# Performance work log

Hardware: AMD Instinct MI355X
Metric: run time of the kernel (lower is better)

Reference implementation:

```python
import jax, jax.numpy as jnp
import numpy as np

N_USERS = 100000
N_ITEMS = 50000
N_NODES = N_USERS + N_ITEMS
NNZ = 4800000
DIM = 64
N_HOPS = 3
EPS = 0.1
PERTURBED = True


def setup_inputs() -> dict:
    key = jax.random.key(0)
    k1, k2, k3, k4, k5 = jax.random.split(key, 5)
    user_embed = jax.random.normal(k1, (N_USERS, DIM), dtype=jnp.float32) * 0.1
    item_embed = jax.random.normal(k2, (N_ITEMS, DIM), dtype=jnp.float32) * 0.1
    adj_rows = jax.random.randint(k3, (NNZ,), 0, N_NODES, dtype=jnp.int32)
    adj_cols = jax.random.randint(k4, (NNZ,), 0, N_NODES, dtype=jnp.int32)
    # scale values ~ 1/avg_degree so repeated propagation stays well-conditioned
    adj_vals = jax.random.uniform(k5, (NNZ,), dtype=jnp.float32) * (1.0 / 32.0)
    return {"user_embed": user_embed, "item_embed": item_embed,
            "adj_rows": adj_rows, "adj_cols": adj_cols, "adj_vals": adj_vals}


def _spmm(rows, cols, vals, x):
    # sparse [N,N] @ dense [N,D] via gather + segment-sum
    msgs = vals[:, None] * x[cols]  # [nnz, D]
    return jax.ops.segment_sum(msgs, rows, num_segments=N_NODES)


def _forward(user_embed, item_embed, adj_rows, adj_cols, adj_vals):
    ego = jnp.concatenate([user_embed, item_embed], axis=0)  # [N, D]
    noise_key = jax.random.key(42)
    all_embeddings = []
    layer_embeddings = ego
    for k in range(N_HOPS):
        ego = _spmm(adj_rows, adj_cols, adj_vals, ego)
        if PERTURBED:
            noise = jax.random.uniform(jax.random.fold_in(noise_key, k), ego.shape, dtype=ego.dtype)
            noise = noise / jnp.linalg.norm(noise, axis=-1, keepdims=True)  # F.normalize dim=-1
            ego = ego + jnp.sign(ego) * noise * EPS
        all_embeddings.append(ego)
        if k == 0:
            layer_embeddings = ego
    all_mean = jnp.mean(jnp.stack(all_embeddings, axis=1), axis=1)  # [N, D]
    user_all, item_all = all_mean[:N_USERS], all_mean[N_USERS:]
    user_layer, item_layer = layer_embeddings[:N_USERS], layer_embeddings[N_USERS:]
    return (user_all, item_all, user_layer, item_layer)


def reference(user_embed, item_embed, adj_rows, adj_cols, adj_vals):
    return _forward(user_embed, item_embed, adj_rows, adj_cols, adj_vals)
```

## Files before the change

### kernel.cpp

```cpp
#include <hip/hip_runtime.h>
#include <stdint.h>

#define N_USERS 100000
#define N_ITEMS 50000
#define N_NODES 150000
#define NNZ     4800000
#define DIM     64
#define NELEM   (N_NODES * DIM)
#define EPS_F   0.1f


#define NBUCK  3072
#define RPB    49
#define BCAP   1856
#define CHUNK  8192
#define NCHUNK 586

#define E_MASK   0x7FFFFFu
#define COL_MASK 0x3FFFFu

typedef unsigned long long ull;

__host__ __device__ inline void threefry2x32_fn(unsigned k0, unsigned k1,
                                                unsigned x0, unsigned x1,
                                                unsigned* o0, unsigned* o1) {
  unsigned ks0 = k0, ks1 = k1, ks2 = k0 ^ k1 ^ 0x1BD11BDAu;
  x0 += ks0; x1 += ks1;
#define TF_ROUND(r) { x0 += x1; x1 = (x1 << (r)) | (x1 >> (32 - (r))); x1 ^= x0; }
  TF_ROUND(13) TF_ROUND(15) TF_ROUND(26) TF_ROUND(6)
  x0 += ks1; x1 += ks2 + 1u;
  TF_ROUND(17) TF_ROUND(29) TF_ROUND(16) TF_ROUND(24)
  x0 += ks2; x1 += ks0 + 2u;
  TF_ROUND(13) TF_ROUND(15) TF_ROUND(26) TF_ROUND(6)
  x0 += ks0; x1 += ks1 + 3u;
  TF_ROUND(17) TF_ROUND(29) TF_ROUND(16) TF_ROUND(24)
  x0 += ks1; x1 += ks2 + 4u;
  TF_ROUND(13) TF_ROUND(15) TF_ROUND(26) TF_ROUND(6)
  x0 += ks2; x1 += ks0 + 5u;
#undef TF_ROUND
  *o0 = x0; *o1 = x1;
}

__global__ void hist_kernel(const int* __restrict__ rows,
                            int* __restrict__ counts) {
  __shared__ int h[NBUCK];
  int c = blockIdx.x, tid = threadIdx.x;
  for (int t = tid; t < NBUCK; t += 256) h[t] = 0;
  __syncthreads();
  int cb = c * CHUNK;
  #pragma unroll 4
  for (int k = 0; k < CHUNK / 256; ++k) {
    int i = cb + k * 256 + tid;
    if (i < NNZ) {
      int r = rows[i];
      atomicAdd(&h[r / RPB], 1);
    }
  }
  __syncthreads();
  for (int t = tid; t < NBUCK; t += 256)
    counts[c * NBUCK + t] = h[t];
}

__global__ void scan_kernel(const int* __restrict__ counts,
                            int* __restrict__ base,
                            int* __restrict__ btot) {
  int b = blockIdx.x * 256 + threadIdx.x;
  int run = 0;
  #pragma unroll 8
  for (int c = 0; c < NCHUNK; ++c) {
    int v = counts[c * NBUCK + b];
    base[c * NBUCK + b] = run;
    run += v;
  }
  btot[b] = run;
}

__global__ void scatter_kernel(const int* __restrict__ rows,
                               const int* __restrict__ cols,
                               const int* __restrict__ base,
                               ull* __restrict__ staging) {
  __shared__ int cur[NBUCK];
  int c = blockIdx.x, tid = threadIdx.x;
  for (int t = tid; t < NBUCK; t += 256) cur[t] = base[c * NBUCK + t];
  __syncthreads();
  int cb = c * CHUNK;
  #pragma unroll 4
  for (int k = 0; k < CHUNK / 256; ++k) {
    int i = cb + k * 256 + tid;
    if (i < NNZ) {
      int r  = rows[i];
      int cc = cols[i];
      int b  = r / RPB;
      int lr = r - b * RPB;
      int p  = atomicAdd(&cur[b], 1);
      if (p < BCAP)
        staging[(long long)b * BCAP + p] =
            ((ull)(unsigned)lr << 41) | ((ull)(unsigned)cc << 23) | (unsigned)i;
    }
  }
}

__global__ void group_sort_kernel(const float* __restrict__ vals,
                                  const int* __restrict__ btot,
                                  ull* __restrict__ staging,
                                  int* __restrict__ cnt,
                                  int* __restrict__ off) {
  __shared__ ull B[BCAP];
  __shared__ int rowcnt[RPB];
  __shared__ int rowoff[RPB + 1];
  __shared__ int rowcur[RPB];
  int b = blockIdx.x, tid = threadIdx.x;
  int tot = btot[b]; if (tot > BCAP) tot = BCAP;
  ull* sg = staging + (long long)b * BCAP;

  for (int t = tid; t < RPB; t += 256) { rowcnt[t] = 0; rowcur[t] = 0; }
  __syncthreads();

  for (int s = tid; s < tot; s += 256) {
    ull v = sg[s];
    atomicAdd(&rowcnt[(int)(v >> 41)], 1);
  }
  __syncthreads();

  if (tid == 0) {
    int run = 0;
    for (int t = 0; t < RPB; ++t) { rowoff[t] = run; run += rowcnt[t]; }
    rowoff[RPB] = run;
  }
  __syncthreads();

  int row0 = b * RPB;
  for (int t = tid; t < RPB; t += 256) {
    int r = row0 + t;
    if (r < N_NODES) { cnt[r] = rowcnt[t]; off[r] = b * BCAP + rowoff[t]; }
  }

  for (int s = tid; s < tot; s += 256) {
    ull v = sg[s];
    int lr = (int)(v >> 41);
    int p = atomicAdd(&rowcur[lr], 1);
    B[rowoff[lr] + p] = v;
  }
  __syncthreads();

  for (int s = tid; s < tot; s += 256) {
    ull v = B[s];
    int lr = (int)(v >> 41);
    unsigned e = (unsigned)(v & E_MASK);
    int lo = rowoff[lr], hi = rowoff[lr + 1];
    int rk = 0;
    for (int j = lo; j < hi; ++j)
      rk += ((unsigned)(B[j] & E_MASK) < e) ? 1 : 0;
    float val = vals[e];
    unsigned col = (unsigned)((v >> 23) & COL_MASK);
    sg[lo + rk] = ((ull)col << 32) | __float_as_uint(val);
  }
}

template <int K>
__global__ void spmm_noise_kernel(const ull* __restrict__ pairs,
                                  const int* __restrict__ cnt,
                                  const int* __restrict__ off,
                                  const float* __restrict__ user_e,
                                  const float* __restrict__ item_e,
                                  const float* __restrict__ src,
                                  float* __restrict__ dst,
                                  float* __restrict__ out_mean,
                                  unsigned key0, unsigned key1) {
  int wid  = threadIdx.x >> 6;
  int lane = threadIdx.x & 63;
  int row  = blockIdx.x * 4 + wid;
  int row_u = __builtin_amdgcn_readfirstlane(row);
  int d = cnt[row_u];
  if (d > 128) d = 128;
  const ull* prow = pairs + off[row_u];

  #define GATHER(c, xout_) do {                                            \
    if (K == 0) {                                                          \
      const float* bp_ = ((c) < N_USERS)                                   \
          ? user_e + (long long)(c) * DIM                                  \
          : item_e + (long long)((c) - N_USERS) * DIM;                     \
      xout_ = bp_[lane];                                                   \
    } else {                                                               \
      xout_ = src[(long long)(c) * DIM + lane];                            \
    }                                                                      \
  } while (0)

  float acc = 0.0f;
  for (int t = 0; t < d; t += 8) {
    int i0 = t,     i1 = t + 1, i2 = t + 2, i3 = t + 3;
    int i4 = t + 4, i5 = t + 5, i6 = t + 6, i7 = t + 7;
    int dm1 = d - 1;
    if (i1 > dm1) i1 = dm1;  if (i2 > dm1) i2 = dm1;  if (i3 > dm1) i3 = dm1;
    if (i4 > dm1) i4 = dm1;  if (i5 > dm1) i5 = dm1;  if (i6 > dm1) i6 = dm1;
    if (i7 > dm1) i7 = dm1;
    ull p0 = prow[i0], p1 = prow[i1], p2 = prow[i2], p3 = prow[i3];
    ull p4 = prow[i4], p5 = prow[i5], p6 = prow[i6], p7 = prow[i7];
    int c0 = (int)(unsigned)(p0 >> 32), c1 = (int)(unsigned)(p1 >> 32);
    int c2 = (int)(unsigned)(p2 >> 32), c3 = (int)(unsigned)(p3 >> 32);
    int c4 = (int)(unsigned)(p4 >> 32), c5 = (int)(unsigned)(p5 >> 32);
    int c6 = (int)(unsigned)(p6 >> 32), c7 = (int)(unsigned)(p7 >> 32);
    float x0, x1, x2, x3, x4, x5, x6, x7;
    GATHER(c0, x0); GATHER(c1, x1); GATHER(c2, x2); GATHER(c3, x3);
    GATHER(c4, x4); GATHER(c5, x5); GATHER(c6, x6); GATHER(c7, x7);
    float v0 = __uint_as_float((unsigned)(p0 & 0xffffffffu));
    float v1 = (t + 1 < d) ? __uint_as_float((unsigned)(p1 & 0xffffffffu)) : 0.0f;
    float v2 = (t + 2 < d) ? __uint_as_float((unsigned)(p2 & 0xffffffffu)) : 0.0f;
    float v3 = (t + 3 < d) ? __uint_as_float((unsigned)(p3 & 0xffffffffu)) : 0.0f;
    float v4 = (t + 4 < d) ? __uint_as_float((unsigned)(p4 & 0xffffffffu)) : 0.0f;
    float v5 = (t + 5 < d) ? __uint_as_float((unsigned)(p5 & 0xffffffffu)) : 0.0f;
    float v6 = (t + 6 < d) ? __uint_as_float((unsigned)(p6 & 0xffffffffu)) : 0.0f;
    float v7 = (t + 7 < d) ? __uint_as_float((unsigned)(p7 & 0xffffffffu)) : 0.0f;
    acc = __fadd_rn(acc, __fmul_rn(v0, x0));
    acc = __fadd_rn(acc, __fmul_rn(v1, x1));
    acc = __fadd_rn(acc, __fmul_rn(v2, x2));
    acc = __fadd_rn(acc, __fmul_rn(v3, x3));
    acc = __fadd_rn(acc, __fmul_rn(v4, x4));
    acc = __fadd_rn(acc, __fmul_rn(v5, x5));
    acc = __fadd_rn(acc, __fmul_rn(v6, x6));
    acc = __fadd_rn(acc, __fmul_rn(v7, x7));
  }
  #undef GATHER

  int i = row * DIM + lane;
  unsigned o0, o1;
  threefry2x32_fn(key0, key1, 0u, (unsigned)i, &o0, &o1);
  unsigned bits = o0 ^ o1;
  float u = __uint_as_float((bits >> 9) | 0x3f800000u) - 1.0f;
  float ss = __fmul_rn(u, u);
  #pragma unroll
  for (int offs = 32; offs >= 1; offs >>= 1)
    ss += __shfl_xor(ss, offs, 64);
  float noise = u / sqrtf(ss);
  float s = (acc > 0.0f) ? 1.0f : ((acc < 0.0f) ? -1.0f : 0.0f);
  float val = __fadd_rn(acc, __fmul_rn(s, __fmul_rn(noise, EPS_F)));

  if (K == 0) {
    dst[i] = val;
    out_mean[i] = val;
  } else if (K == 1) {
    dst[i] = val;
    out_mean[i] = __fadd_rn(out_mean[i], val);
  } else {
    out_mean[i] = __fadd_rn(out_mean[i], val) / 3.0f;
  }
}

extern "C" void kernel_launch(void* const* d_in, const int* in_sizes, int n_in,
                              void* d_out, int out_size, void* d_ws, size_t ws_size,
                              hipStream_t stream) {
  const float* user_e = (const float*)d_in[0];
  const float* item_e = (const float*)d_in[1];
  const int*   rows   = (const int*)d_in[2];
  const int*   cols   = (const int*)d_in[3];
  const float* vals   = (const float*)d_in[4];

  float* out_mean  = (float*)d_out;
  float* out_layer = (float*)d_out + NELEM;

  char* w = (char*)d_ws;
  ull*   staging = (ull*)w;
  int*   counts  = (int*)(w + 45613056);
  int*   basep   = (int*)(w + 52813824);
  int*   btot    = (int*)(w + 60014592);
  int*   cnt     = (int*)(w + 60026880);
  int*   off     = (int*)(w + 60626880);
  float* ego     = (float*)(w + 61226880);

  unsigned hk0[3], hk1[3];
  for (int k = 0; k < 3; ++k)
    threefry2x32_fn(0u, 42u, 0u, (unsigned)k, &hk0[k], &hk1[k]);

  const int BT = 256;
  const unsigned row_blocks = N_NODES / 4;

  hist_kernel<<<NCHUNK, BT, 0, stream>>>(rows, counts);
  scan_kernel<<<NBUCK / BT, BT, 0, stream>>>(counts, basep, btot);
  scatter_kernel<<<NCHUNK, BT, 0, stream>>>(rows, cols, basep, staging);
  group_sort_kernel<<<NBUCK, BT, 0, stream>>>(vals, btot, staging, cnt, off);

  spmm_noise_kernel<0><<<row_blocks, BT, 0, stream>>>(
      staging, cnt, off, user_e, item_e, nullptr, out_layer, out_mean, hk0[0], hk1[0]);
  spmm_noise_kernel<1><<<row_blocks, BT, 0, stream>>>(
      staging, cnt, off, nullptr, nullptr, out_layer, ego, out_mean, hk0[1], hk1[1]);
  spmm_noise_kernel<2><<<row_blocks, BT, 0, stream>>>(
      staging, cnt, off, nullptr, nullptr, ego, nullptr, out_mean, hk0[2], hk1[2]);
}
```

Measured before the change: 910.0 us.

## Fuse histogram, scan and scatter into one kernel using global atomic bucket offsets

The separate histogram, per-bucket scan and scatter kernels become a single kernel. Each chunk block builds its local bucket histogram in shared memory, reserves space in each bucket with one global atomicAdd on a zeroed bucket counter, then scatters entries. This drops two kernel launches and the counts/base arrays with their scan traffic. In exchange, the order of entries inside a bucket is no longer deterministic across chunks, which relies on the later per-bucket sort to restore order. Block size also rises to 1024 threads.

```diff
diff --git a/kernel.cpp b/kernel.cpp
--- a/kernel.cpp
+++ b/kernel.cpp
@@ -41,58 +41,38 @@
   *o0 = x0; *o1 = x1;
 }
 
-__global__ void hist_kernel(const int* __restrict__ rows,
-                            int* __restrict__ counts) {
+__global__ __launch_bounds__(1024)
+void scatter_kernel(const int* __restrict__ rows,
+                    const int* __restrict__ cols,
+                    int* __restrict__ gcnt,
+                    ull* __restrict__ staging) {
   __shared__ int h[NBUCK];
   int c = blockIdx.x, tid = threadIdx.x;
-  for (int t = tid; t < NBUCK; t += 256) h[t] = 0;
+  for (int t = tid; t < NBUCK; t += 1024) h[t] = 0;
   __syncthreads();
   int cb = c * CHUNK;
-  #pragma unroll 4
-  for (int k = 0; k < CHUNK / 256; ++k) {
-    int i = cb + k * 256 + tid;
-    if (i < NNZ) {
-      int r = rows[i];
-      atomicAdd(&h[r / RPB], 1);
-    }
-  }
-  __syncthreads();
-  for (int t = tid; t < NBUCK; t += 256)
-    counts[c * NBUCK + t] = h[t];
-}
-
-__global__ void scan_kernel(const int* __restrict__ counts,
-                            int* __restrict__ base,
-                            int* __restrict__ btot) {
-  int b = blockIdx.x * 256 + threadIdx.x;
-  int run = 0;
-  #pragma unroll 8
-  for (int c = 0; c < NCHUNK; ++c) {
-    int v = counts[c * NBUCK + b];
-    base[c * NBUCK + b] = run;
-    run += v;
-  }
-  btot[b] = run;
-}
-
-__global__ void scatter_kernel(const int* __restrict__ rows,
-                               const int* __restrict__ cols,
-                               const int* __restrict__ base,
-                               ull* __restrict__ staging) {
-  __shared__ int cur[NBUCK];
-  int c = blockIdx.x, tid = threadIdx.x;
-  for (int t = tid; t < NBUCK; t += 256) cur[t] = base[c * NBUCK + t];
-  __syncthreads();
-  int cb = c * CHUNK;
-  #pragma unroll 4
-  for (int k = 0; k < CHUNK / 256; ++k) {
-    int i = cb + k * 256 + tid;
+  #pragma unroll
+  for (int k = 0; k < CHUNK / 1024; ++k) {
+    int i = cb + k * 1024 + tid;
+    if (i < NNZ)
+      atomicAdd(&h[rows[i] / RPB], 1);
+  }
+  __syncthreads();
+  for (int t = tid; t < NBUCK; t += 1024) {
+    int n = h[t];
+    if (n > 0)
+      h[t] = atomicAdd(&gcnt[t], n);
+  }
+  __syncthreads();
+  #pragma unroll
+  for (int k = 0; k < CHUNK / 1024; ++k) {
+    int i = cb + k * 1024 + tid;
     if (i < NNZ) {
       int r  = rows[i];
       int cc = cols[i];
       int b  = r / RPB;
       int lr = r - b * RPB;
-      int p  = atomicAdd(&cur[b], 1);
+      int p  = atomicAdd(&h[b], 1);
       if (p < BCAP)
         staging[(long long)b * BCAP + p] =
             ((ull)(unsigned)lr << 41) | ((ull)(unsigned)cc << 23) | (unsigned)i;
@@ -260,29 +240,25 @@
 
   char* w = (char*)d_ws;
   ull*   staging = (ull*)w;
-  int*   counts  = (int*)(w + 45613056);
-  int*   basep   = (int*)(w + 52813824);
-  int*   btot    = (int*)(w + 60014592);
-  int*   cnt     = (int*)(w + 60026880);
-  int*   off     = (int*)(w + 60626880);
-  float* ego     = (float*)(w + 61226880);
+  int*   gcnt    = (int*)(w + 45613056);
+  int*   cnt     = (int*)(w + 45625344);
+  int*   off     = (int*)(w + 46225344);
+  float* ego     = (float*)(w + 46825344);
 
   unsigned hk0[3], hk1[3];
   for (int k = 0; k < 3; ++k)
     threefry2x32_fn(0u, 42u, 0u, (unsigned)k, &hk0[k], &hk1[k]);
 
-  const int BT = 256;
   const unsigned row_blocks = N_NODES / 4;
 
-  hist_kernel<<<NCHUNK, BT, 0, stream>>>(rows, counts);
-  scan_kernel<<<NBUCK / BT, BT, 0, stream>>>(counts, basep, btot);
-  scatter_kernel<<<NCHUNK, BT, 0, stream>>>(rows, cols, basep, staging);
-  group_sort_kernel<<<NBUCK, BT, 0, stream>>>(vals, btot, staging, cnt, off);
-
-  spmm_noise_kernel<0><<<row_blocks, BT, 0, stream>>>(
+  hipMemsetAsync(gcnt, 0, NBUCK * sizeof(int), stream);
+  scatter_kernel<<<NCHUNK, 1024, 0, stream>>>(rows, cols, gcnt, staging);
+  group_sort_kernel<<<NBUCK, 256, 0, stream>>>(vals, gcnt, staging, cnt, off);
+
+  spmm_noise_kernel<0><<<row_blocks, 256, 0, stream>>>(
       staging, cnt, off, user_e, item_e, nullptr, out_layer, out_mean, hk0[0], hk1[0]);
-  spmm_noise_kernel<1><<<row_blocks, BT, 0, stream>>>(
+  spmm_noise_kernel<1><<<row_blocks, 256, 0, stream>>>(
       staging, cnt, off, nullptr, nullptr, out_layer, ego, out_mean, hk0[1], hk1[1]);
-  spmm_noise_kernel<2><<<row_blocks, BT, 0, stream>>>(
+  spmm_noise_kernel<2><<<row_blocks, 256, 0, stream>>>(
       staging, cnt, off, nullptr, nullptr, ego, nullptr, out_mean, hk0[2], hk1[2]);
 }
```

New measurement: 846.9 us. 1.07x faster.
